# Kernel tuning notes

Measured on AMD Instinct MI355X. Metric: run time of the kernel, lower is better.

The kernel has to match this reference:

```python
import jax, jax.numpy as jnp
import numpy as np
from jax import lax

EPS = 1e-5

def _conv(x, w, b, stride, pad):
    y = lax.conv_general_dilated(x, w, (stride, stride), ((pad, pad), (pad, pad)),
                                 dimension_numbers=('NCHW', 'OIHW', 'NCHW'))
    return y + b[None, :, None, None]

def _deconv(x, w, b):
    # torch ConvTranspose2d(k=4, s=2, p=1): weight (Cin, Cout, 4, 4)
    w2 = jnp.flip(w, (2, 3)).transpose(1, 0, 2, 3)  # OIHW for forward conv
    y = lax.conv_general_dilated(x, w2, (1, 1), ((2, 2), (2, 2)),
                                 lhs_dilation=(2, 2),
                                 dimension_numbers=('NCHW', 'OIHW', 'NCHW'))
    return y + b[None, :, None, None]

def _bn(x, g, b):
    m = jnp.mean(x, axis=(0, 2, 3), keepdims=True)
    v = jnp.mean((x - m) ** 2, axis=(0, 2, 3), keepdims=True)
    return g[None, :, None, None] * (x - m) * lax.rsqrt(v + EPS) + b[None, :, None, None]

def setup_inputs() -> dict:
    key = jax.random.key(0)
    ks = jax.random.split(key, 16)
    f32 = jnp.float32
    def w(k, shape):
        return (jax.random.normal(k, shape, f32) * 0.05)
    inp = {
        'x': jax.random.uniform(ks[0], (32, 1, 512, 512), f32),
        'w1': w(ks[1], (16, 1, 4, 4)),  'b1': jnp.zeros((16,), f32), 'g1': jnp.ones((16,), f32), 'be1': jnp.zeros((16,), f32),
        'w2': w(ks[2], (16, 16, 4, 4)), 'b2': jnp.zeros((16,), f32), 'g2': jnp.ones((16,), f32), 'be2': jnp.zeros((16,), f32),
        'w3': w(ks[3], (4, 16, 4, 4)),  'b3': jnp.zeros((4,), f32),  'g3': jnp.ones((4,), f32),  'be3': jnp.zeros((4,), f32),
        'wpre': w(ks[4], (2, 4, 1, 1)), 'bpre': jnp.zeros((2,), f32),
        'codebook': w(ks[5], (256, 2)),
        'wpost': w(ks[6], (4, 2, 1, 1)), 'bpost': jnp.zeros((4,), f32),
        'wd1': w(ks[7], (4, 16, 4, 4)),  'bd1': jnp.zeros((16,), f32), 'g4': jnp.ones((16,), f32), 'be4': jnp.zeros((16,), f32),
        'wd2': w(ks[8], (16, 16, 4, 4)), 'bd2': jnp.zeros((16,), f32), 'g5': jnp.ones((16,), f32), 'be5': jnp.zeros((16,), f32),
        'wd3': w(ks[9], (16, 1, 4, 4)),  'bd3': jnp.zeros((1,), f32),
    }
    return inp

def _forward(x, w1, b1, g1, be1, w2, b2, g2, be2, w3, b3, g3, be3,
             wpre, bpre, codebook, wpost, bpost,
             wd1, bd1, g4, be4, wd2, bd2, g5, be5, wd3, bd3):
    # encoder: three stride-2 convs with BN + ReLU
    h = jax.nn.relu(_bn(_conv(x, w1, b1, 2, 1), g1, be1))
    h = jax.nn.relu(_bn(_conv(h, w2, b2, 2, 1), g2, be2))
    h = jax.nn.relu(_bn(_conv(h, w3, b3, 2, 1), g3, be3))
    q = _conv(h, wpre, bpre, 1, 0)          # [B, 2, H/8, W/8]
    B, C, Hq, Wq = q.shape
    qf = q.transpose(0, 2, 3, 1).reshape(B * Hq * Wq, C)   # [N, 2]
    # squared Euclidean distances to codebook (argmin equals cdist argmin)
    d2 = (jnp.sum(qf * qf, -1, keepdims=True)
          - 2.0 * qf @ codebook.T
          + jnp.sum(codebook * codebook, -1)[None, :])     # [N, 256]
    idx = jnp.argmin(d2, axis=-1)
    quant = codebook[idx]                                   # gather [N, 2]
    commitment_loss = jnp.mean((lax.stop_gradient(quant) - qf) ** 2)
    codebook_loss = jnp.mean((quant - lax.stop_gradient(qf)) ** 2)
    qout = qf + lax.stop_gradient(quant - qf)               # straight-through
    qout = qout.reshape(B, Hq, Wq, C).transpose(0, 3, 1, 2)
    d = _conv(qout, wpost, bpost, 1, 0)
    d = jax.nn.relu(_bn(_deconv(d, wd1, bd1), g4, be4))
    d = jax.nn.relu(_bn(_deconv(d, wd2, bd2), g5, be5))
    out = jax.nn.sigmoid(_deconv(d, wd3, bd3))
    recon = jnp.mean((x - out) ** 2)
    total = 1.0 * recon + codebook_loss + 0.2 * commitment_loss
    return out, total

def reference(x, w1, b1, g1, be1, w2, b2, g2, be2, w3, b3, g3, be3,
              wpre, bpre, codebook, wpost, bpost,
              wd1, bd1, g4, be4, wd2, bd2, g5, be5, wd3, bd3):
    return _forward(x, w1, b1, g1, be1, w2, b2, g2, be2, w3, b3, g3, be3,
                    wpre, bpre, codebook, wpost, bpost,
                    wd1, bd1, g4, be4, wd2, bd2, g5, be5, wd3, bd3)
```

## Files before the change

kernel.cpp:

```cpp
#include <hip/hip_runtime.h>
#include <hip/hip_bf16.h>
#include <math.h>

using bf16 = __hip_bfloat16;

__device__ __forceinline__ float b2f(bf16 v) { return __bfloat162float(v); }
__device__ __forceinline__ float ldv(const void* p, size_t i, int m) {
  return m ? b2f(((const bf16*)p)[i]) : ((const float*)p)[i];
}

struct D2 { double s, s2; };

__device__ __forceinline__ void block_stats1(float v, D2* slot) {
  float v2 = v * v;
#pragma unroll
  for (int o = 32; o; o >>= 1) { v += __shfl_down(v, o, 64); v2 += __shfl_down(v2, o, 64); }
  __shared__ float a1[4], a2[4];
  int lane = threadIdx.x & 63, w = threadIdx.x >> 6;
  if (lane == 0) { a1[w] = v; a2[w] = v2; }
  __syncthreads();
  if (threadIdx.x == 0) {
    slot->s  = (double)a1[0] + a1[1] + a1[2] + a1[3];
    slot->s2 = (double)a2[0] + a2[1] + a2[2] + a2[3];
  }
}

__device__ __forceinline__ void block_stats1d4(const double* v, const double* vq, D2* base, int NB, int bx) {
  __shared__ double q1[16], q2[16];
  int lane = threadIdx.x & 63, w = threadIdx.x >> 6;
#pragma unroll
  for (int k = 0; k < 4; k++) {
    double s = v[k], s2 = vq[k];
#pragma unroll
    for (int o = 32; o; o >>= 1) { s += __shfl_down(s, o, 64); s2 += __shfl_down(s2, o, 64); }
    if (lane == 0) { q1[k * 4 + w] = s; q2[k * 4 + w] = s2; }
  }
  __syncthreads();
  if (threadIdx.x < 4) {
    int k = threadIdx.x;
    base[k * NB + bx].s  = q1[k * 4] + q1[k * 4 + 1] + q1[k * 4 + 2] + q1[k * 4 + 3];
    base[k * NB + bx].s2 = q2[k * 4] + q2[k * 4 + 1] + q2[k * 4 + 2] + q2[k * 4 + 3];
  }
}

__device__ __forceinline__ void block_sum1(float v, double* slot) {
#pragma unroll
  for (int o = 32; o; o >>= 1) v += __shfl_down(v, o, 64);
  __shared__ float a1[4];
  int lane = threadIdx.x & 63, w = threadIdx.x >> 6;
  if (lane == 0) a1[w] = v;
  __syncthreads();
  if (threadIdx.x == 0) *slot = (double)a1[0] + a1[1] + a1[2] + a1[3];
}

__device__ __forceinline__ void block_stats16(const float* vs, const float* vq, D2* base, int NB, int bx) {
  __shared__ float s1[64], s2[64];
  int lane = threadIdx.x & 63, w = threadIdx.x >> 6;
#pragma unroll
  for (int co = 0; co < 16; co++) {
    float v = vs[co], v2 = vq[co];
#pragma unroll
    for (int o = 32; o; o >>= 1) { v += __shfl_down(v, o, 64); v2 += __shfl_down(v2, o, 64); }
    if (lane == 0) { s1[co * 4 + w] = v; s2[co * 4 + w] = v2; }
  }
  __syncthreads();
  if (threadIdx.x < 16) {
    int co = threadIdx.x;
    base[co * NB + bx].s  = (double)s1[co * 4] + s1[co * 4 + 1] + s1[co * 4 + 2] + s1[co * 4 + 3];
    base[co * NB + bx].s2 = (double)s2[co * 4] + s2[co * 4 + 1] + s2[co * 4 + 2] + s2[co * 4 + 3];
  }
}

__global__ void prep_k(const unsigned* __restrict__ xw, int* __restrict__ MODE,
                       const void* w1, const void* b1, const void* w2, const void* b2,
                       const void* w3, const void* b3, const void* wpre, const void* bpre,
                       const void* cbk, const void* wpost, const void* bpost,
                       const void* wd1, const void* bd1, const void* wd2, const void* bd2,
                       const void* wd3, const void* bd3,
                       const void* g1, const void* be1, const void* g2, const void* be2,
                       const void* g3, const void* be3, const void* g4, const void* be4,
                       const void* g5, const void* be5,
                       float* __restrict__ PF, double* __restrict__ PD) {
  int t = threadIdx.x;
  __shared__ int smode;
  {
    unsigned lo = xw[t] & 0xFFFFu;
    int inr = (lo >= 0x3000u && lo < 0x4000u) ? 1 : 0;
    unsigned long long b = __ballot(inr);
    __shared__ int cnt[4];
    if ((t & 63) == 0) cnt[t >> 6] = __popcll(b);
    __syncthreads();
    if (t == 0) { smode = (cnt[0] + cnt[1] + cnt[2] + cnt[3] >= 128) ? 1 : 0; *MODE = smode; }
    __syncthreads();
  }
  int m = smode;
  for (int i = t; i < 256; i += 256) PF[i] = ldv(w1, i, m);
  if (t < 16) PF[256 + t] = ldv(b1, t, m);
  for (int i = t; i < 4096; i += 256) {
    int cig = i >> 10, tap = (i >> 6) & 15, c4 = (i >> 4) & 3, co = i & 15;
    PF[272 + i] = ldv(w2, co * 256 + (cig * 4 + c4) * 16 + tap, m);
  }
  if (t < 16) PF[4368 + t] = ldv(b2, t, m);
  for (int i = t; i < 1024; i += 256) {
    int co = i >> 6, ci = (i >> 4) & 3, tap = i & 15;
    PF[4384 + i] = ldv(wd1, ci * 256 + co * 16 + tap, m);
  }
  for (int i = t; i < 1024; i += 256) {
    int ci = i >> 8, tap = (i >> 4) & 15, co = i & 15;
    PF[14368 + i] = ldv(wd1, ci * 256 + co * 16 + tap, m);
  }
  if (t < 16) PF[5408 + t] = ldv(bd1, t, m);
  for (int i = t; i < 4096; i += 256) {
    int co = i >> 8, ci = (i >> 4) & 15, tap = i & 15;
    PF[5424 + i] = ldv(wd2, ci * 256 + co * 16 + tap, m);
  }
  for (int i = t; i < 4096; i += 256) {
    int ci = i >> 8, tap = (i >> 4) & 15, co = i & 15;
    PF[10272 + i] = ldv(wd2, ci * 256 + co * 16 + tap, m);
  }
  if (t < 16) PF[9520 + t] = ldv(bd2, t, m);
  for (int i = t; i < 256; i += 256) PF[9536 + i] = ldv(wd3, i, m);
  {
    int tap = t >> 4, ci = t & 15;
    PF[10016 + t] = ldv(wd3, ci * 16 + tap, m);
  }
  if (t == 0) PF[9792] = ldv(bd3, 0, m);
  if (t < 16) {
    PF[9856 + t] = ldv(g1, t, m);  PF[9872 + t] = ldv(be1, t, m);
    PF[9888 + t] = ldv(g2, t, m);  PF[9904 + t] = ldv(be2, t, m);
    PF[9952 + t] = ldv(g4, t, m);  PF[9968 + t] = ldv(be4, t, m);
    PF[9984 + t] = ldv(g5, t, m);  PF[10000 + t] = ldv(be5, t, m);
  }
  if (t < 4) { PF[9920 + t] = ldv(g3, t, m); PF[9936 + t] = ldv(be3, t, m); }
  for (int i = t; i < 1024; i += 256) PD[i] = ldv(w3, i, m);
  if (t < 4) PD[1024 + t] = ldv(b3, t, m);
  if (t < 8) PD[1028 + t] = ldv(wpre, t, m);
  if (t < 2) PD[1036 + t] = ldv(bpre, t, m);
  for (int i = t; i < 512; i += 256) PD[1040 + i] = ldv(cbk, i, m);
  if (t < 8) PD[1552 + t] = ldv(wpost, t, m);
  if (t < 4) PD[1560 + t] = ldv(bpost, t, m);
}

__global__ __launch_bounds__(256) void bn_reduce_k(const D2* __restrict__ part, int NB,
                                                   double* __restrict__ stD, float* __restrict__ stF,
                                                   const float* __restrict__ gb, double invN) {
  int c = blockIdx.x;
  double s = 0, s2 = 0;
  for (int i = threadIdx.x; i < NB; i += 256) { D2 p = part[c * NB + i]; s += p.s; s2 += p.s2; }
#pragma unroll
  for (int o = 32; o; o >>= 1) { s += __shfl_down(s, o, 64); s2 += __shfl_down(s2, o, 64); }
  __shared__ double l1[4], l2[4];
  int lane = threadIdx.x & 63, w = threadIdx.x >> 6;
  if (lane == 0) { l1[w] = s; l2[w] = s2; }
  __syncthreads();
  if (threadIdx.x == 0) {
    double S = l1[0] + l1[1] + l1[2] + l1[3], Q = l2[0] + l2[1] + l2[2] + l2[3];
    double mu = S * invN, var = Q * invN - mu * mu;
    if (var < 0) var = 0;
    double sc = (double)gb[c] / sqrt(var + 1e-5);
    double sh = (double)gb[16 + c] - mu * sc;
    stD[c] = sc; stD[16 + c] = sh;
    stF[c] = (float)sc; stF[16 + c] = (float)sh;
  }
}

__global__ __launch_bounds__(256) void conv1_t(const void* __restrict__ x, const float* __restrict__ PF,
                                               float* __restrict__ y, D2* __restrict__ part,
                                               const int* modep) {
  const int m = *modep;
  __shared__ float sx[10 * 132];
  int t = threadIdx.x;
  int bx = blockIdx.x;
  int b = bx >> 8, r = bx & 255, tY = r >> 2, tX = r & 3;
  int iy0 = 8 * tY - 1, ix0e = 128 * tX - 2;
  size_t xb = (size_t)b * 262144;
  for (int i = t; i < 660; i += 256) {
    int ry = i / 66, px = i - ry * 66;
    int gy = iy0 + ry, gx = ix0e + 2 * px;
    float a = 0.f, b2 = 0.f;
    if ((unsigned)gy < 512u && (unsigned)gx < 512u) {
      size_t base = xb + (size_t)gy * 512 + gx;
      if (m) {
        unsigned u = *(const unsigned*)((const bf16*)x + base);
        a  = __uint_as_float(u << 16);
        b2 = __uint_as_float(u & 0xFFFF0000u);
      } else {
        float2 f = *(const float2*)((const float*)x + base);
        a = f.x; b2 = f.y;
      }
    }
    int s = ry * 132 + 2 * px;
    sx[s] = a; sx[s + 1] = b2;
  }
  __syncthreads();
  int tyy = t >> 6, txx = t & 63;
  int oy = tY * 4 + tyy, ox = tX * 64 + txx;
  float acc[16];
#pragma unroll
  for (int co = 0; co < 16; co++) acc[co] = PF[256 + co];
  int ly = 2 * tyy, lx = 2 * txx + 1;
#pragma unroll
  for (int ky = 0; ky < 4; ky++) {
#pragma unroll
    for (int kx = 0; kx < 4; kx++) {
      float v = sx[(ly + ky) * 132 + lx + kx];
#pragma unroll
      for (int co = 0; co < 16; co++) acc[co] = fmaf(v, PF[co * 16 + ky * 4 + kx], acc[co]);
    }
  }
  size_t pix = (size_t)b * 65536 + (size_t)(oy * 256 + ox);
  *(float4*)(y + 0 * 8388608 + pix * 4) = make_float4(acc[0],  acc[1],  acc[2],  acc[3]);
  *(float4*)(y + 1 * 8388608 + pix * 4) = make_float4(acc[4],  acc[5],  acc[6],  acc[7]);
  *(float4*)(y + 2 * 8388608 + pix * 4) = make_float4(acc[8],  acc[9],  acc[10], acc[11]);
  *(float4*)(y + 3 * 8388608 + pix * 4) = make_float4(acc[12], acc[13], acc[14], acc[15]);
  float vq_[16];
#pragma unroll
  for (int co = 0; co < 16; co++) vq_[co] = acc[co] * acc[co];
  block_stats16(acc, vq_, part, 8192, bx);
}

__device__ __forceinline__ float4 aff_relu4(float4 v, float4 sc, float4 sh) {
  v.x = fmaxf(fmaf(v.x, sc.x, sh.x), 0.f);
  v.y = fmaxf(fmaf(v.y, sc.y, sh.y), 0.f);
  v.z = fmaxf(fmaf(v.z, sc.z, sh.z), 0.f);
  v.w = fmaxf(fmaf(v.w, sc.w, sh.w), 0.f);
  return v;
}

__global__ __launch_bounds__(256, 6) void conv2_t(const float* __restrict__ h1, const float* __restrict__ PF,
                                                  const float* __restrict__ aff, float* __restrict__ h2,
                                                  D2* __restrict__ part) {
  __shared__ float4 su4[1224];
  int t = threadIdx.x, ty = t >> 4, tx = t & 15;
  int bx = blockIdx.x, bb = bx >> 6, r = bx & 63, tY = r >> 3, tX = r & 7;
  int oy = tY * 16 + ty, ox = tX * 16 + tx;
  int iy0 = 32 * tY - 1, ix0 = 32 * tX - 1;
  const float* W2 = PF + 272;
  const float4* A4 = (const float4*)aff;
  int goff[5], soff[5];
#pragma unroll
  for (int k = 0; k < 5; k++) {
    int i = t + k * 256;
    goff[k] = -1; soff[k] = -1;
    if (i < 1156) {
      int riy = i / 34, rix = i - riy * 34;
      int gy = iy0 + riy, gx = ix0 + rix;
      soff[k] = (rix & 1) * 612 + riy * 18 + (rix >> 1);
      if ((unsigned)gy < 256u && (unsigned)gx < 256u) goff[k] = (gy * 256 + gx) * 4;
    }
  }
  const float* pb = h1 + (size_t)bb * 262144;
  float4 rv[5];
#pragma unroll
  for (int k = 0; k < 5; k++) {
    float4 v = make_float4(0.f, 0.f, 0.f, 0.f);
    if (goff[k] >= 0) v = *(const float4*)(pb + goff[k]);
    rv[k] = v;
  }
  float acc[16];
#pragma unroll
  for (int co = 0; co < 16; co++) acc[co] = PF[4368 + co];
#pragma unroll
  for (int g = 0; g < 4; g++) {
    float4 SC = A4[g], SH = A4[4 + g];
    __syncthreads();
#pragma unroll
    for (int k = 0; k < 5; k++) {
      if (soff[k] >= 0) {
        float4 v = make_float4(0.f, 0.f, 0.f, 0.f);
        if (goff[k] >= 0) v = aff_relu4(rv[k], SC, SH);
        su4[soff[k]] = v;
      }
    }
    __syncthreads();
    if (g < 3) {
      const float* pg = pb + (size_t)(g + 1) * 8388608;
#pragma unroll
      for (int k = 0; k < 5; k++) {
        float4 v = make_float4(0.f, 0.f, 0.f, 0.f);
        if (goff[k] >= 0) v = *(const float4*)(pg + goff[k]);
        rv[k] = v;
      }
    }
    const float* wg = W2 + g * 1024;
    int base = 2 * ty * 18 + tx;
#pragma unroll
    for (int ky = 0; ky < 4; ky++) {
#pragma unroll
      for (int kx = 0; kx < 4; kx++) {
        float4 vv = su4[(kx & 1) * 612 + ky * 18 + (kx >> 1) + base];
        const float* wt = wg + (ky * 4 + kx) * 64;
#pragma unroll
        for (int co = 0; co < 16; co++) {
          float s0 = fmaf(vv.x, wt[co], acc[co]);
          float s1 = fmaf(vv.y, wt[16 + co], s0);
          float s2 = fmaf(vv.z, wt[32 + co], s1);
          acc[co] = fmaf(vv.w, wt[48 + co], s2);
        }
      }
    }
  }
  float vq_[16];
#pragma unroll
  for (int co = 0; co < 16; co++) {
    h2[((size_t)(bb * 16 + co) * 128 + oy) * 128 + ox] = acc[co];
    vq_[co] = acc[co] * acc[co];
  }
  block_stats16(acc, vq_, part, 2048, bx);
}

__global__ __launch_bounds__(256) void conv3_k(const float* __restrict__ h2, const double* __restrict__ PD,
                                               const float* __restrict__ aff, double* __restrict__ c3,
                                               D2* __restrict__ part) {
  int idx = blockIdx.x * 256 + threadIdx.x;
  int b = idx >> 12, rem = idx & 4095, oy = rem >> 6, ox = rem & 63;
  double a0 = PD[1024], a1 = PD[1025], a2 = PD[1026], a3 = PD[1027];
  int iy0 = 2 * oy - 1, ix0 = 2 * ox - 1;
  for (int ci = 0; ci < 16; ci++) {
    const float* ib = h2 + (size_t)(b * 16 + ci) * 16384;
    float sc = aff[ci], sh = aff[16 + ci];
    const double* wr = PD + ci * 16;
#pragma unroll
    for (int ky = 0; ky < 4; ky++) {
      int iy = iy0 + ky;
      if ((unsigned)iy < 128u) {
        const float* row = ib + iy * 128;
#pragma unroll
        for (int kx = 0; kx < 4; kx++) {
          int ix = ix0 + kx;
          if ((unsigned)ix < 128u) {
            double v = (double)fmaxf(fmaf(row[ix], sc, sh), 0.f);
            int tp = ky * 4 + kx;
            a0 = fma(v, wr[tp], a0);
            a1 = fma(v, wr[256 + tp], a1);
            a2 = fma(v, wr[512 + tp], a2);
            a3 = fma(v, wr[768 + tp], a3);
          }
        }
      }
    }
  }
  size_t cb = (size_t)b * 16384 + rem;
  c3[cb] = a0; c3[cb + 4096] = a1; c3[cb + 8192] = a2; c3[cb + 12288] = a3;
  double vs[4] = {a0, a1, a2, a3};
  double vq[4] = {a0 * a0, a1 * a1, a2 * a2, a3 * a3};
  block_stats1d4(vs, vq, part, 512, blockIdx.x);
}

__global__ __launch_bounds__(256) void vq_k(const double* __restrict__ c3, const double* __restrict__ PD,
                                            const double* __restrict__ stD2, float* __restrict__ d0,
                                            double* __restrict__ vp) {
  __shared__ double cb[512];
  for (int i = threadIdx.x; i < 512; i += 256) cb[i] = PD[1040 + i];
  __syncthreads();
  int pix = blockIdx.x * 256 + threadIdx.x;
  int b = pix >> 12, rem = pix & 4095;
  const double* hb = c3 + (size_t)b * 16384 + rem;
  double q0 = PD[1036], q1 = PD[1037];
#pragma unroll
  for (int ci = 0; ci < 4; ci++) {
    double v = fma(hb[ci * 4096], stD2[ci], stD2[16 + ci]);
    if (v < 0) v = 0;
    q0 = fma(v, PD[1028 + ci], q0);
    q1 = fma(v, PD[1032 + ci], q1);
  }
  int best = 0;
  double bd = 1e300;
  for (int k = 0; k < 256; k++) {
    double dx = q0 - cb[2 * k], dy = q1 - cb[2 * k + 1];
    double d = dx * dx + dy * dy;
    if (d < bd) { bd = d; best = k; }
  }
  double c0 = cb[2 * best], c1 = cb[2 * best + 1];
  double e0 = q0 - c0, e1 = q1 - c1;
  float* ob = d0 + (size_t)b * 16384 + rem;
#pragma unroll
  for (int c = 0; c < 4; c++)
    ob[c * 4096] = (float)(PD[1560 + c] + PD[1552 + 2 * c] * c0 + PD[1552 + 2 * c + 1] * c1);
  double v = e0 * e0 + e1 * e1;
#pragma unroll
  for (int o = 32; o; o >>= 1) v += __shfl_down(v, o, 64);
  __shared__ double l1[4];
  int lane = threadIdx.x & 63, w = threadIdx.x >> 6;
  if (lane == 0) l1[w] = v;
  __syncthreads();
  if (threadIdx.x == 0) vp[blockIdx.x] = l1[0] + l1[1] + l1[2] + l1[3];
}

__global__ __launch_bounds__(256) void deconv1_k(const float* __restrict__ d0, const float* __restrict__ PF,
                                                 float* __restrict__ d1, D2* __restrict__ part) {
  int phase = blockIdx.y, a = phase >> 1, bc = phase & 1;
  int idx = blockIdx.x * 256 + threadIdx.x;
  int b = idx >> 12, rem = idx & 4095, qy = rem >> 6, qx = rem & 63;
  const float* WT = PF + 14368;
  float acc[16];
#pragma unroll
  for (int co = 0; co < 16; co++) acc[co] = PF[5408 + co];
  const float* hb = d0 + (size_t)b * 16384;
#pragma unroll
  for (int t2y = 0; t2y < 2; t2y++) {
    int iy = qy + a - t2y;
    if ((unsigned)iy < 64u) {
      int kyo = (1 - a + 2 * t2y) * 4;
#pragma unroll
      for (int t2x = 0; t2x < 2; t2x++) {
        int ix = qx + bc - t2x;
        if ((unsigned)ix < 64u) {
          int tap = kyo + (1 - bc + 2 * t2x);
          int off = iy * 64 + ix;
#pragma unroll
          for (int ci = 0; ci < 4; ci++) {
            float v = hb[ci * 4096 + off];
            const float* wt = WT + ci * 256 + tap * 16;
#pragma unroll
            for (int co = 0; co < 16; co++) acc[co] = fmaf(v, wt[co], acc[co]);
          }
        }
      }
    }
  }
  int oy = 2 * qy + a, ox = 2 * qx + bc;
  size_t pix = (size_t)b * 16384 + (size_t)(oy * 128 + ox);
  *(float4*)(d1 + 0 * 2097152 + pix * 4) = make_float4(acc[0],  acc[1],  acc[2],  acc[3]);
  *(float4*)(d1 + 1 * 2097152 + pix * 4) = make_float4(acc[4],  acc[5],  acc[6],  acc[7]);
  *(float4*)(d1 + 2 * 2097152 + pix * 4) = make_float4(acc[8],  acc[9],  acc[10], acc[11]);
  *(float4*)(d1 + 3 * 2097152 + pix * 4) = make_float4(acc[12], acc[13], acc[14], acc[15]);
  float vq_[16];
#pragma unroll
  for (int co = 0; co < 16; co++) vq_[co] = acc[co] * acc[co];
  block_stats16(acc, vq_, part, 2048, blockIdx.y * 512 + blockIdx.x);
}

__global__ __launch_bounds__(256) void deconv2_t(const float* __restrict__ d1, const float* __restrict__ PF,
                                                 const float* __restrict__ aff, float* __restrict__ d2,
                                                 D2* __restrict__ part) {
  __shared__ float su[16 * 324];
  int t = threadIdx.x, py = t >> 4, px = t & 15;
  int bx = blockIdx.x, bb = bx >> 6, r = bx & 63, tY = r >> 3, tX = r & 7;
  int iy0 = 16 * tY - 1, ix0 = 16 * tX - 1;
  const float4* A4 = (const float4*)aff;
  for (int i = t; i < 1296; i += 256) {
    int g = i / 324, rr = i - g * 324;
    int riy = rr / 18, rix = rr - riy * 18;
    int gy = iy0 + riy, gx = ix0 + rix;
    float4 v = make_float4(0.f, 0.f, 0.f, 0.f);
    if ((unsigned)gy < 128u && (unsigned)gx < 128u)
      v = aff_relu4(*(const float4*)(d1 + (size_t)g * 2097152 +
                                     ((size_t)bb * 16384 + (size_t)(gy * 128 + gx)) * 4),
                    A4[g], A4[4 + g]);
    int s0 = g * 1296 + rr;
    su[s0] = v.x; su[s0 + 324] = v.y; su[s0 + 648] = v.z; su[s0 + 972] = v.w;
  }
  __syncthreads();
  const float* WT = PF + 10272;
  float vs[16], vq[16];
#pragma unroll
  for (int co = 0; co < 16; co++) { vs[co] = 0.f; vq[co] = 0.f; }
#pragma unroll
  for (int a = 0; a < 2; a++) {
#pragma unroll
    for (int bc = 0; bc < 2; bc++) {
      float acc[16];
#pragma unroll
      for (int co = 0; co < 16; co++) acc[co] = PF[9520 + co];
      int base = (py + a) * 18 + (px + bc);
      for (int ci = 0; ci < 16; ci++) {
        const float* sb = su + ci * 324 + base;
        float v00 = sb[0], v01 = sb[1], v10 = sb[18], v11 = sb[19];
        const float* wci = WT + ci * 256;
        const float* w00p = wci + (((3 - a) * 4 + (3 - bc)) << 4);
        const float* w01p = wci + (((3 - a) * 4 + (1 - bc)) << 4);
        const float* w10p = wci + (((1 - a) * 4 + (3 - bc)) << 4);
        const float* w11p = wci + (((1 - a) * 4 + (1 - bc)) << 4);
#pragma unroll
        for (int co = 0; co < 16; co++) {
          float s0 = fmaf(v00, w00p[co], acc[co]);
          float s1 = fmaf(v01, w01p[co], s0);
          float s2 = fmaf(v10, w10p[co], s1);
          acc[co] = fmaf(v11, w11p[co], s2);
        }
      }
      int oy = 32 * tY + 2 * py + a, ox = 32 * tX + 2 * px + bc;
      float4* dst = (float4*)(d2 + ((size_t)bb * 65536 + (size_t)oy * 256 + ox) * 16);
      dst[0] = make_float4(acc[0],  acc[1],  acc[2],  acc[3]);
      dst[1] = make_float4(acc[4],  acc[5],  acc[6],  acc[7]);
      dst[2] = make_float4(acc[8],  acc[9],  acc[10], acc[11]);
      dst[3] = make_float4(acc[12], acc[13], acc[14], acc[15]);
#pragma unroll
      for (int co = 0; co < 16; co++) {
        vs[co] += acc[co];
        vq[co] = fmaf(acc[co], acc[co], vq[co]);
      }
    }
  }
  block_stats16(vs, vq, part, 2048, bx);
}

__device__ __forceinline__ int swz(int p, int g) {
  int s = p * 4 + (g ^ (p & 3));
  return s ^ (((p >> 2) & 1) << 2);
}

__device__ __forceinline__ float4 aff_relu(float4 v, float4 sc, float4 sh) {
  v.x = fmaxf(fmaf(v.x, sc.x, sh.x), 0.f);
  v.y = fmaxf(fmaf(v.y, sc.y, sh.y), 0.f);
  v.z = fmaxf(fmaf(v.z, sc.z, sh.z), 0.f);
  v.w = fmaxf(fmaf(v.w, sc.w, sh.w), 0.f);
  return v;
}

__device__ __forceinline__ void dot4(float& a, float4 v, float4 w) {
  a = fmaf(v.x, w.x, a); a = fmaf(v.y, w.y, a);
  a = fmaf(v.z, w.z, a); a = fmaf(v.w, w.w, a);
}

__global__ __launch_bounds__(256, 4) void deconv3_t(const float* __restrict__ d2, const float* __restrict__ PF,
                                                    const float* __restrict__ aff, const void* __restrict__ x,
                                                    void* __restrict__ outp, double* __restrict__ rp,
                                                    const int* __restrict__ modep) {
  const int m = *modep;
  __shared__ float4 sd4[1296];
  int t = threadIdx.x;
  int bx = blockIdx.x;
  int b = bx >> 8, r = bx & 255, tY = r >> 4, tX = r & 15;
  int iy0 = 16 * tY - 1, ix0 = 16 * tX - 1;
  const float4* A4 = (const float4*)aff;
  float4 SC0 = A4[0], SC1 = A4[1], SC2 = A4[2], SC3 = A4[3];
  float4 SH0 = A4[4], SH1 = A4[5], SH2 = A4[6], SH3 = A4[7];
  const float* db = d2 + (size_t)b * 1048576;
  for (int p = t; p < 324; p += 256) {
    int riy = p / 18, rix = p - riy * 18;
    int gy = iy0 + riy, gx = ix0 + rix;
    float4 v0, v1, v2, v3;
    if ((unsigned)gy < 256u && (unsigned)gx < 256u) {
      const float4* s = (const float4*)(db + ((size_t)gy * 256 + gx) * 16);
      v0 = aff_relu(s[0], SC0, SH0);
      v1 = aff_relu(s[1], SC1, SH1);
      v2 = aff_relu(s[2], SC2, SH2);
      v3 = aff_relu(s[3], SC3, SH3);
    } else {
      v0 = v1 = v2 = v3 = make_float4(0.f, 0.f, 0.f, 0.f);
    }
    sd4[swz(p, 0)] = v0; sd4[swz(p, 1)] = v1; sd4[swz(p, 2)] = v2; sd4[swz(p, 3)] = v3;
  }
  __syncthreads();

  int lx = t & 15, ly = t >> 4;
  float bias = PF[9792];
  float a00 = bias, a01 = bias, a10 = bias, a11 = bias;
  const float* WT = PF + 10016;
  int p00 = ly * 18 + lx;
#define TAPW(ky, kx) (*(const float4*)(WT + ((ky) * 4 + (kx)) * 16 + (g << 2)))
#pragma unroll
  for (int g = 0; g < 4; g++) {
    float4 w33 = TAPW(3, 3), w31 = TAPW(3, 1), w32 = TAPW(3, 2), w30 = TAPW(3, 0);
    float4 w13 = TAPW(1, 3), w11 = TAPW(1, 1), w12 = TAPW(1, 2), w10 = TAPW(1, 0);
    float4 w23 = TAPW(2, 3), w21 = TAPW(2, 1), w22 = TAPW(2, 2), w20 = TAPW(2, 0);
    float4 w03 = TAPW(0, 3), w01 = TAPW(0, 1), w02 = TAPW(0, 2), w00 = TAPW(0, 0);
    float4 v;
    v = sd4[swz(p00, g)];      dot4(a00, v, w33);
    v = sd4[swz(p00 + 1, g)];  dot4(a00, v, w31); dot4(a01, v, w32);
    v = sd4[swz(p00 + 2, g)];  dot4(a01, v, w30);
    v = sd4[swz(p00 + 18, g)]; dot4(a00, v, w13); dot4(a10, v, w23);
    v = sd4[swz(p00 + 19, g)]; dot4(a00, v, w11); dot4(a01, v, w12); dot4(a10, v, w21); dot4(a11, v, w22);
    v = sd4[swz(p00 + 20, g)]; dot4(a01, v, w10); dot4(a11, v, w20);
    v = sd4[swz(p00 + 36, g)]; dot4(a10, v, w03);
    v = sd4[swz(p00 + 37, g)]; dot4(a10, v, w01); dot4(a11, v, w02);
    v = sd4[swz(p00 + 38, g)]; dot4(a11, v, w00);
  }
#undef TAPW

  int oy = 32 * tY + 2 * ly, ox = 32 * tX + 2 * lx;
  size_t ob = (size_t)b * 262144 + (size_t)oy * 512 + ox;
  float o0 = 1.f / (1.f + expf(-a00));
  float o1 = 1.f / (1.f + expf(-a01));
  float o2 = 1.f / (1.f + expf(-a10));
  float o3 = 1.f / (1.f + expf(-a11));
  if (m) {
    bf16* op = (bf16*)outp;
    op[ob] = __float2bfloat16(o0);       op[ob + 1] = __float2bfloat16(o1);
    op[ob + 512] = __float2bfloat16(o2); op[ob + 513] = __float2bfloat16(o3);
  } else {
    float* op = (float*)outp;
    op[ob] = o0;       op[ob + 1] = o1;
    op[ob + 512] = o2; op[ob + 513] = o3;
  }
  float d0_ = ldv(x, ob, m) - o0;
  float d1_ = ldv(x, ob + 1, m) - o1;
  float d2_ = ldv(x, ob + 512, m) - o2;
  float d3_ = ldv(x, ob + 513, m) - o3;
  float ds = fmaf(d0_, d0_, fmaf(d1_, d1_, fmaf(d2_, d2_, d3_ * d3_)));
  block_sum1(ds, rp + bx);
}

__global__ __launch_bounds__(256) void finalize_k(const double* __restrict__ vp, const double* __restrict__ rp,
                                                  void* outp, const int* modep) {
  double s = 0, rr = 0;
  for (int i = threadIdx.x; i < 512; i += 256) s += vp[i];
  for (int i = threadIdx.x; i < 8192; i += 256) rr += rp[i];
#pragma unroll
  for (int o = 32; o; o >>= 1) { s += __shfl_down(s, o, 64); rr += __shfl_down(rr, o, 64); }
  __shared__ double l1[4], l2[4];
  int lane = threadIdx.x & 63, w = threadIdx.x >> 6;
  if (lane == 0) { l1[w] = s; l2[w] = rr; }
  __syncthreads();
  if (threadIdx.x == 0) {
    double S = l1[0] + l1[1] + l1[2] + l1[3], R = l2[0] + l2[1] + l2[2] + l2[3];
    double total = R * (1.0 / 8388608.0) + 1.2 * (S * (1.0 / 262144.0));
    if (*modep) ((bf16*)outp)[8388608] = __float2bfloat16((float)total);
    else        ((float*)outp)[8388608] = (float)total;
  }
}

extern "C" void kernel_launch(void* const* d_in, const int* in_sizes, int n_in,
                              void* d_out, int out_size, void* d_ws, size_t ws_size,
                              hipStream_t stream) {
  const void* x    = d_in[0];
  const void* w1   = d_in[1];  const void* b1  = d_in[2];
  const void* g1   = d_in[3];  const void* be1 = d_in[4];
  const void* w2   = d_in[5];  const void* b2  = d_in[6];
  const void* g2   = d_in[7];  const void* be2 = d_in[8];
  const void* w3   = d_in[9];  const void* b3  = d_in[10];
  const void* g3   = d_in[11]; const void* be3 = d_in[12];
  const void* wpre = d_in[13]; const void* bpre= d_in[14];
  const void* cbk  = d_in[15];
  const void* wpost= d_in[16]; const void* bpost= d_in[17];
  const void* wd1  = d_in[18]; const void* bd1 = d_in[19];
  const void* g4   = d_in[20]; const void* be4 = d_in[21];
  const void* wd2  = d_in[22]; const void* bd2 = d_in[23];
  const void* g5   = d_in[24]; const void* be5 = d_in[25];
  const void* wd3  = d_in[26]; const void* bd3 = d_in[27];

  char* ws = (char*)d_ws;
  int*    MODE = (int*)ws;
  float*  STF  = (float*)(ws + 1024);
  double* STD  = (double*)(ws + 4096);
  float*  PF   = (float*)(ws + 8192);
  double* PD   = (double*)(ws + 73728);
  D2*     P1   = (D2*)(ws + 131072);
  D2*     P2   = (D2*)(ws + 2228224);
  D2*     P3   = (D2*)(ws + 2752512);
  D2*     P4   = (D2*)(ws + 2785280);
  D2*     P5   = (D2*)(ws + 3309568);
  double* VP   = (double*)(ws + 3833856);
  double* RP   = (double*)(ws + 3837952);
  char* HB = ws + 6291456;
  float*    H1  = (float*)HB;
  float*    H2  = (float*)(HB + 134217728);
  double*   C3  = (double*)HB;
  float*    D0  = (float*)(HB + 165675008);
  float*    D1  = (float*)HB;
  float*    D2T = (float*)(HB + 33554432);

  prep_k<<<1, 256, 0, stream>>>((const unsigned*)x, MODE,
                                w1, b1, w2, b2, w3, b3, wpre, bpre, cbk, wpost, bpost,
                                wd1, bd1, wd2, bd2, wd3, bd3,
                                g1, be1, g2, be2, g3, be3, g4, be4, g5, be5, PF, PD);

  conv1_t<<<8192, 256, 0, stream>>>(x, PF, H1, P1, MODE);
  bn_reduce_k<<<16, 256, 0, stream>>>(P1, 8192, STD + 0, STF + 0, PF + 9856, 1.0 / 2097152.0);

  conv2_t<<<2048, 256, 0, stream>>>(H1, PF, STF + 0, H2, P2);
  bn_reduce_k<<<16, 256, 0, stream>>>(P2, 2048, STD + 32, STF + 32, PF + 9888, 1.0 / 524288.0);

  conv3_k<<<512, 256, 0, stream>>>(H2, PD, STF + 32, C3, P3);
  bn_reduce_k<<<4, 256, 0, stream>>>(P3, 512, STD + 64, STF + 64, PF + 9920, 1.0 / 131072.0);

  vq_k<<<512, 256, 0, stream>>>(C3, PD, STD + 64, D0, VP);

  deconv1_k<<<dim3(512, 4), 256, 0, stream>>>(D0, PF, D1, P4);
  bn_reduce_k<<<16, 256, 0, stream>>>(P4, 2048, STD + 96, STF + 96, PF + 9952, 1.0 / 524288.0);

  deconv2_t<<<2048, 256, 0, stream>>>(D1, PF, STF + 96, D2T, P5);
  bn_reduce_k<<<16, 256, 0, stream>>>(P5, 2048, STD + 128, STF + 128, PF + 9984, 1.0 / 2097152.0);

  deconv3_t<<<8192, 256, 0, stream>>>(D2T, PF, STF + 128, x, d_out, RP, MODE);
  finalize_k<<<1, 256, 0, stream>>>(VP, RP, d_out, MODE);
}
```

Before: 539.1 us.

## Recompute conv1 inside conv2 instead of materializing H1 activation

```diff
diff --git a/kernel.cpp b/kernel.cpp
--- a/kernel.cpp
+++ b/kernel.cpp
@@ -165,8 +165,7 @@
 }
 
 __global__ __launch_bounds__(256) void conv1_t(const void* __restrict__ x, const float* __restrict__ PF,
-                                               float* __restrict__ y, D2* __restrict__ part,
-                                               const int* modep) {
+                                               D2* __restrict__ part, const int* modep) {
   const int m = *modep;
   __shared__ float sx[10 * 132];
   int t = threadIdx.x;
@@ -194,7 +193,6 @@
   }
   __syncthreads();
   int tyy = t >> 6, txx = t & 63;
-  int oy = tY * 4 + tyy, ox = tX * 64 + txx;
   float acc[16];
 #pragma unroll
   for (int co = 0; co < 16; co++) acc[co] = PF[256 + co];
@@ -208,11 +206,6 @@
       for (int co = 0; co < 16; co++) acc[co] = fmaf(v, PF[co * 16 + ky * 4 + kx], acc[co]);
     }
   }
-  size_t pix = (size_t)b * 65536 + (size_t)(oy * 256 + ox);
-  *(float4*)(y + 0 * 8388608 + pix * 4) = make_float4(acc[0],  acc[1],  acc[2],  acc[3]);
-  *(float4*)(y + 1 * 8388608 + pix * 4) = make_float4(acc[4],  acc[5],  acc[6],  acc[7]);
-  *(float4*)(y + 2 * 8388608 + pix * 4) = make_float4(acc[8],  acc[9],  acc[10], acc[11]);
-  *(float4*)(y + 3 * 8388608 + pix * 4) = make_float4(acc[12], acc[13], acc[14], acc[15]);
   float vq_[16];
 #pragma unroll
   for (int co = 0; co < 16; co++) vq_[co] = acc[co] * acc[co];
@@ -227,61 +220,85 @@
   return v;
 }
 
-__global__ __launch_bounds__(256, 6) void conv2_t(const float* __restrict__ h1, const float* __restrict__ PF,
+__global__ __launch_bounds__(256, 4) void conv2_t(const void* __restrict__ x, const float* __restrict__ PF,
                                                   const float* __restrict__ aff, float* __restrict__ h2,
-                                                  D2* __restrict__ part) {
+                                                  D2* __restrict__ part, const int* modep) {
+  const int m = *modep;
+  __shared__ float sxx[70 * 72];
   __shared__ float4 su4[1224];
   int t = threadIdx.x, ty = t >> 4, tx = t & 15;
   int bx = blockIdx.x, bb = bx >> 6, r = bx & 63, tY = r >> 3, tX = r & 7;
   int oy = tY * 16 + ty, ox = tX * 16 + tx;
   int iy0 = 32 * tY - 1, ix0 = 32 * tX - 1;
+  int xy0 = 64 * tY - 3, xx0e = 64 * tX - 4;
+  size_t xb = (size_t)bb * 262144;
+  for (int i = t; i < 2520; i += 256) {
+    int ry = i / 36, px = i - ry * 36;
+    int gy = xy0 + ry, gx = xx0e + 2 * px;
+    float a = 0.f, b2 = 0.f;
+    if ((unsigned)gy < 512u && (unsigned)gx < 512u) {
+      size_t base = xb + (size_t)gy * 512 + gx;
+      if (m) {
+        unsigned u = *(const unsigned*)((const bf16*)x + base);
+        a  = __uint_as_float(u << 16);
+        b2 = __uint_as_float(u & 0xFFFF0000u);
+      } else {
+        float2 f = *(const float2*)((const float*)x + base);
+        a = f.x; b2 = f.y;
+      }
+    }
+    int s = ry * 72 + 2 * px;
+    sxx[s] = a; sxx[s + 1] = b2;
+  }
+  int rsoff[5], rbase[5];
+#pragma unroll
+  for (int k = 0; k < 5; k++) {
+    int i = t + k * 256;
+    rsoff[k] = -1; rbase[k] = -1;
+    if (i < 1156) {
+      int riy = i / 34, rix = i - riy * 34;
+      int hy = iy0 + riy, hx = ix0 + rix;
+      rsoff[k] = (rix & 1) * 612 + riy * 18 + (rix >> 1);
+      if ((unsigned)hy < 256u && (unsigned)hx < 256u) rbase[k] = 2 * riy * 72 + 2 * rix + 1;
+    }
+  }
   const float* W2 = PF + 272;
   const float4* A4 = (const float4*)aff;
-  int goff[5], soff[5];
-#pragma unroll
-  for (int k = 0; k < 5; k++) {
-    int i = t + k * 256;
-    goff[k] = -1; soff[k] = -1;
-    if (i < 1156) {
-      int riy = i / 34, rix = i - riy * 34;
-      int gy = iy0 + riy, gx = ix0 + rix;
-      soff[k] = (rix & 1) * 612 + riy * 18 + (rix >> 1);
-      if ((unsigned)gy < 256u && (unsigned)gx < 256u) goff[k] = (gy * 256 + gx) * 4;
-    }
-  }
-  const float* pb = h1 + (size_t)bb * 262144;
-  float4 rv[5];
-#pragma unroll
-  for (int k = 0; k < 5; k++) {
-    float4 v = make_float4(0.f, 0.f, 0.f, 0.f);
-    if (goff[k] >= 0) v = *(const float4*)(pb + goff[k]);
-    rv[k] = v;
-  }
   float acc[16];
 #pragma unroll
   for (int co = 0; co < 16; co++) acc[co] = PF[4368 + co];
+  __syncthreads();
 #pragma unroll
   for (int g = 0; g < 4; g++) {
     float4 SC = A4[g], SH = A4[4 + g];
+    float B0 = PF[256 + 4 * g], B1 = PF[257 + 4 * g], B2 = PF[258 + 4 * g], B3 = PF[259 + 4 * g];
+    const float* w1g = PF + g * 64;
+    if (g) __syncthreads();
+#pragma unroll
+    for (int k = 0; k < 5; k++) {
+      if (rsoff[k] >= 0) {
+        float4 v = make_float4(0.f, 0.f, 0.f, 0.f);
+        if (rbase[k] >= 0) {
+          float a0 = B0, a1 = B1, a2 = B2, a3 = B3;
+          const float* xbse = sxx + rbase[k];
+#pragma unroll
+          for (int ky = 0; ky < 4; ky++) {
+#pragma unroll
+            for (int kx = 0; kx < 4; kx++) {
+              float xv = xbse[ky * 72 + kx];
+              int tp = ky * 4 + kx;
+              a0 = fmaf(xv, w1g[tp], a0);
+              a1 = fmaf(xv, w1g[16 + tp], a1);
+              a2 = fmaf(xv, w1g[32 + tp], a2);
+              a3 = fmaf(xv, w1g[48 + tp], a3);
+            }
+          }
+          v = aff_relu4(make_float4(a0, a1, a2, a3), SC, SH);
+        }
+        su4[rsoff[k]] = v;
+      }
+    }
     __syncthreads();
-#pragma unroll
-    for (int k = 0; k < 5; k++) {
-      if (soff[k] >= 0) {
-        float4 v = make_float4(0.f, 0.f, 0.f, 0.f);
-        if (goff[k] >= 0) v = aff_relu4(rv[k], SC, SH);
-        su4[soff[k]] = v;
-      }
-    }
-    __syncthreads();
-    if (g < 3) {
-      const float* pg = pb + (size_t)(g + 1) * 8388608;
-#pragma unroll
-      for (int k = 0; k < 5; k++) {
-        float4 v = make_float4(0.f, 0.f, 0.f, 0.f);
-        if (goff[k] >= 0) v = *(const float4*)(pg + goff[k]);
-        rv[k] = v;
-      }
-    }
     const float* wg = W2 + g * 1024;
     int base = 2 * ty * 18 + tx;
 #pragma unroll
@@ -645,7 +662,6 @@
   double* VP   = (double*)(ws + 3833856);
   double* RP   = (double*)(ws + 3837952);
   char* HB = ws + 6291456;
-  float*    H1  = (float*)HB;
   float*    H2  = (float*)(HB + 134217728);
   double*   C3  = (double*)HB;
   float*    D0  = (float*)(HB + 165675008);
@@ -657,10 +673,10 @@
                                 wd1, bd1, wd2, bd2, wd3, bd3,
                                 g1, be1, g2, be2, g3, be3, g4, be4, g5, be5, PF, PD);
 
-  conv1_t<<<8192, 256, 0, stream>>>(x, PF, H1, P1, MODE);
+  conv1_t<<<8192, 256, 0, stream>>>(x, PF, P1, MODE);
   bn_reduce_k<<<16, 256, 0, stream>>>(P1, 8192, STD + 0, STF + 0, PF + 9856, 1.0 / 2097152.0);
 
-  conv2_t<<<2048, 256, 0, stream>>>(H1, PF, STF + 0, H2, P2);
+  conv2_t<<<2048, 256, 0, stream>>>(x, PF, STF + 0, H2, P2, MODE);
   bn_reduce_k<<<16, 256, 0, stream>>>(P2, 2048, STD + 32, STF + 32, PF + 9888, 1.0 / 524288.0);
 
   conv3_k<<<512, 256, 0, stream>>>(H2, PD, STF + 32, C3, P3);
```

Measured after the change: 575.9 us. 6.8% more time.
